# Kernel optimization log

Hardware: AMD Instinct MI355X
Metric: run time of the kernel (lower is better)

The kernel has to match this reference:

```python
import jax, jax.numpy as jnp
import numpy as np

N = 100000
E = 1600000
IN_CH = 128
HEADS = 4
OUT_CH = 32


def setup_inputs() -> dict:
    key = jax.random.key(0)
    k1, k2, k3, k4, k5, k6 = jax.random.split(key, 6)
    x = jax.random.normal(k1, (N, IN_CH), dtype=jnp.float32)
    edge_attr = jax.random.normal(k2, (E,), dtype=jnp.float32)
    edge_index = jax.random.randint(k3, (2, E), 0, N, dtype=jnp.int64)
    # xavier-uniform-ish parameter init
    def xavier(k, shape):
        fan_in, fan_out = shape[-1], shape[-2] if len(shape) > 1 else shape[-1]
        lim = jnp.sqrt(6.0 / (fan_in + fan_out)).astype(jnp.float32)
        return jax.random.uniform(k, shape, jnp.float32, -lim, lim)
    lin_w = xavier(k4, (HEADS * OUT_CH, IN_CH))       # nn.Linear weight [out,in]
    lin_edge_w = xavier(k5, (HEADS * OUT_CH, 1))      # [out,1]
    att = xavier(k6, (1, HEADS, 3 * OUT_CH))
    return {"x": x, "edge_attr": edge_attr, "edge_index": edge_index,
            "lin_w": lin_w, "lin_edge_w": lin_edge_w, "att": att}


def reference(x, edge_attr, edge_index, lin_w, lin_edge_w, att):
    n = x.shape[0]
    # node transform: [N, H, C]
    xh = (x @ lin_w.T).reshape(n, HEADS, OUT_CH)
    # edge transform: [E, H, C]
    eh = (edge_attr[:, None] @ lin_edge_w.T).reshape(-1, HEADS, OUT_CH)
    row, col = edge_index[0], edge_index[1]
    # split att into source/dest/edge parts to avoid materializing cat([x_i,x_j,e])
    att_i, att_j, att_e = jnp.split(att, 3, axis=-1)  # each [1, H, C]
    # per-edge attention logits: [E, H]
    alpha = ((xh[row] * att_i).sum(-1)
             + (xh[col] * att_j).sum(-1)
             + (eh * att_e).sum(-1))
    alpha = jax.nn.leaky_relu(alpha, negative_slope=0.2)
    # segment softmax over destination node (row)
    amax = jax.ops.segment_max(alpha, row, num_segments=n)           # [N, H]
    amax = jnp.where(jnp.isfinite(amax), amax, 0.0)
    ex = jnp.exp(alpha - amax[row])
    den = jax.ops.segment_sum(ex, row, num_segments=n)               # [N, H]
    alpha = ex / (den[row] + 1e-16)
    # weighted message scatter-add: [N, H, C]
    out = jax.ops.segment_sum(alpha[..., None] * xh[col], row, num_segments=n)
    # concat heads
    return out.reshape(n, HEADS * OUT_CH)
```

## Files before the change

### kernel.cpp

```cpp
#include <hip/hip_runtime.h>

#define HEADS 4
#define OUT_CH 32
#define HC 128
#define INC 128
#define CAP 48

typedef __attribute__((ext_vector_type(8))) short bfrag;
typedef __attribute__((ext_vector_type(4))) float ffrag;

union U16 { uint4 u; bfrag f; };

__device__ __forceinline__ unsigned short f2bf(float f) {
  unsigned int u = __float_as_uint(f);
  unsigned int r = (u + 0x7FFFu + ((u >> 16) & 1u)) >> 16;
  return (unsigned short)r;
}

__global__ void prep_kernel(const float* __restrict__ W,
                            const float* __restrict__ lew,
                            const float* __restrict__ att,
                            unsigned short* __restrict__ Wb,
                            float* __restrict__ ce) {
  int tid = threadIdx.x;
#pragma unroll
  for (int t = 0; t < 64; t++) {
    int idx = tid + t * 256;
    Wb[idx] = f2bf(W[idx]);
  }
  if (tid < HEADS) {
    float s = 0.f;
    for (int c = 0; c < OUT_CH; ++c)
      s += lew[tid * OUT_CH + c] * att[tid * 96 + 2 * OUT_CH + c];
    ce[tid] = s;
  }
}

#define APITCH 136
__global__ __launch_bounds__(256) void gemm_build(
    const float* __restrict__ x, const unsigned short* __restrict__ Wb,
    const float* __restrict__ att, const int* __restrict__ ei,
    const float* __restrict__ ea, unsigned short* __restrict__ xhb,
    float* __restrict__ si, float* __restrict__ sj, int* __restrict__ cnt,
    unsigned int* __restrict__ slots, int nrows, int E, int G) {
  __shared__ unsigned short Als[4][16 * APITCH];

  if (blockIdx.x >= G) {
    int e = (blockIdx.x - G) * 256 + threadIdx.x;
    if (e < E) {
      int r = ei[e];
      int c = ei[E + e];
      unsigned int u = __float_as_uint(ea[e]);
      unsigned int word = ((u + 0x10000u) & 0xFFFE0000u) | (unsigned int)c;
      int pos = atomicAdd(&cnt[r], 1);
      if (pos < CAP) slots[(size_t)r * CAP + pos] = word;
    }
    return;
  }

  const int tid = threadIdx.x;
  const int wid = tid >> 6;
  const int lane = tid & 63;
  const int row0 = blockIdx.x * 64 + wid * 16;
  if (row0 >= nrows) return;
  unsigned short* As = &Als[wid][0];

#pragma unroll
  for (int t = 0; t < 8; t++) {
    int idx = t * 64 + lane;
    int r = idx >> 5;
    int q = idx & 31;
    int gr = row0 + r;
    float4 v = make_float4(0.f, 0.f, 0.f, 0.f);
    if (gr < nrows) v = ((const float4*)x)[(size_t)gr * 32 + q];
    unsigned int p0 = ((unsigned int)f2bf(v.y) << 16) | f2bf(v.x);
    unsigned int p1 = ((unsigned int)f2bf(v.w) << 16) | f2bf(v.z);
    *(uint2*)&As[r * APITCH + q * 4] = make_uint2(p0, p1);
  }

  const int m15 = lane & 15;
  const int g = lane >> 4;

  ffrag acc[8];
#pragma unroll
  for (int t = 0; t < 8; t++) acc[t] = (ffrag){0.f, 0.f, 0.f, 0.f};

#pragma unroll
  for (int ks = 0; ks < 4; ks++) {
    U16 a;
    a.u = *(const uint4*)&As[m15 * APITCH + ks * 32 + g * 8];
#pragma unroll
    for (int nt = 0; nt < 8; nt++) {
      U16 b;
      b.u = *(const uint4*)&Wb[(size_t)(nt * 16 + m15) * 128 + ks * 32 + g * 8];
      acc[nt] = __builtin_amdgcn_mfma_f32_16x16x32_bf16(a.f, b.f, acc[nt],
                                                        0, 0, 0);
    }
  }

  float ai[8], aj[8];
#pragma unroll
  for (int t = 0; t < 8; t++) {
    int h = t >> 1, c = (t & 1) * 16 + m15;
    ai[t] = att[h * 96 + c];
    aj[t] = att[h * 96 + 32 + c];
  }
#pragma unroll
  for (int reg = 0; reg < 4; reg++) {
    float ph_i[4], ph_j[4];
#pragma unroll
    for (int h = 0; h < 4; h++) {
      ph_i[h] = acc[2 * h][reg] * ai[2 * h] + acc[2 * h + 1][reg] * ai[2 * h + 1];
      ph_j[h] = acc[2 * h][reg] * aj[2 * h] + acc[2 * h + 1][reg] * aj[2 * h + 1];
    }
#pragma unroll
    for (int off = 8; off >= 1; off >>= 1) {
#pragma unroll
      for (int h = 0; h < 4; h++) {
        ph_i[h] += __shfl_down(ph_i[h], off, 16);
        ph_j[h] += __shfl_down(ph_j[h], off, 16);
      }
    }
    int gr = row0 + g * 4 + reg;
    if (m15 == 0 && gr < nrows) {
#pragma unroll
      for (int h = 0; h < 4; h++) {
        si[(size_t)gr * 4 + h] = ph_i[h];
        sj[(size_t)gr * 4 + h] = ph_j[h];
      }
    }
  }

#pragma unroll
  for (int t = 0; t < 8; t++) {
#pragma unroll
    for (int reg = 0; reg < 4; reg++) {
      int r = g * 4 + reg;
      int n = t * 16 + m15;
      As[r * 128 + n] = f2bf(acc[t][reg]);
    }
  }
  const uint4* src = (const uint4*)As;
#pragma unroll
  for (int t = 0; t < 4; t++) {
    int idx = t * 64 + lane;
    int r = idx >> 4, q = idx & 15;
    int gr = row0 + r;
    if (gr < nrows) ((uint4*)(xhb + (size_t)gr * 128))[q] = src[idx];
  }
}

__global__ __launch_bounds__(256) void gather_kernel(
    const int* __restrict__ cnt, const unsigned int* __restrict__ slots,
    const float* __restrict__ si, const float* __restrict__ sj,
    const float* __restrict__ ce, const unsigned short* __restrict__ xhb,
    float* __restrict__ out, int n) {
  __shared__ int cls[4][CAP];
  __shared__ float wls[4][4][CAP];

  int wid = threadIdx.x >> 6;
  int node = blockIdx.x * 4 + wid;
  if (node >= n) return;
  int lane = threadIdx.x & 63;
  int h = lane >> 4;

  int m = cnt[node];
  if (m > CAP) m = CAP;

  float4 si4 = *(const float4*)(si + (size_t)node * 4);
  float4 ce4 = *(const float4*)ce;

  if (lane < CAP) {
    int c = 0;
    float w0 = 0.f, w1 = 0.f, w2 = 0.f, w3 = 0.f;
    if (lane < m) {
      unsigned int word = slots[(size_t)node * CAP + lane];
      c = word & 0x1FFFF;
      float eaf = __uint_as_float(word & 0xFFFE0000u);
      float4 sjv = *(const float4*)(sj + (size_t)c * 4);
      float t0 = si4.x + sjv.x + eaf * ce4.x;
      float t1 = si4.y + sjv.y + eaf * ce4.y;
      float t2 = si4.z + sjv.z + eaf * ce4.z;
      float t3 = si4.w + sjv.w + eaf * ce4.w;
      t0 = t0 > 0.f ? t0 : 0.2f * t0;
      t1 = t1 > 0.f ? t1 : 0.2f * t1;
      t2 = t2 > 0.f ? t2 : 0.2f * t2;
      t3 = t3 > 0.f ? t3 : 0.2f * t3;
      w0 = __expf(t0);
      w1 = __expf(t1);
      w2 = __expf(t2);
      w3 = __expf(t3);
    }
    cls[wid][lane] = c;
    wls[wid][0][lane] = w0;
    wls[wid][1][lane] = w1;
    wls[wid][2][lane] = w2;
    wls[wid][3][lane] = w3;
  }

  const unsigned short* xb = xhb + lane * 2;
  float acc0 = 0.f, acc1 = 0.f, wsum = 0.f;
  for (int k = 0; k < m; k += 4) {
    int4 cc = *(const int4*)&cls[wid][k];
    float4 wv = *(const float4*)&wls[wid][h][k];
    unsigned int x0 = *(const unsigned int*)(xb + (size_t)cc.x * 128);
    unsigned int x1 = *(const unsigned int*)(xb + (size_t)cc.y * 128);
    unsigned int x2 = *(const unsigned int*)(xb + (size_t)cc.z * 128);
    unsigned int x3 = *(const unsigned int*)(xb + (size_t)cc.w * 128);
    acc0 += wv.x * __uint_as_float(x0 << 16) +
            wv.y * __uint_as_float(x1 << 16) +
            wv.z * __uint_as_float(x2 << 16) +
            wv.w * __uint_as_float(x3 << 16);
    acc1 += wv.x * __uint_as_float(x0 & 0xFFFF0000u) +
            wv.y * __uint_as_float(x1 & 0xFFFF0000u) +
            wv.z * __uint_as_float(x2 & 0xFFFF0000u) +
            wv.w * __uint_as_float(x3 & 0xFFFF0000u);
    wsum += wv.x + wv.y + wv.z + wv.w;
  }

  float inv = 1.0f / (wsum + 1e-16f);
  float2 o;
  o.x = acc0 * inv;
  o.y = acc1 * inv;
  *(float2*)(out + (size_t)node * HC + lane * 2) = o;
}

extern "C" void kernel_launch(void* const* d_in, const int* in_sizes, int n_in,
                              void* d_out, int out_size, void* d_ws,
                              size_t ws_size, hipStream_t stream) {
  const float* x = (const float*)d_in[0];
  const float* edge_attr = (const float*)d_in[1];
  const int* ei = (const int*)d_in[2];
  const float* lin_w = (const float*)d_in[3];
  const float* lew = (const float*)d_in[4];
  const float* att = (const float*)d_in[5];
  float* out = (float*)d_out;

  const int N = in_sizes[0] / INC;
  const int E = in_sizes[1];

  unsigned int* slots = (unsigned int*)d_ws;
  unsigned short* xhb = (unsigned short*)(slots + (size_t)N * CAP);
  float* si = (float*)(xhb + (size_t)N * 128);
  float* sj = si + (size_t)N * 4;
  float* ce = sj + (size_t)N * 4;
  unsigned short* Wb = (unsigned short*)(ce + 16);
  int* cnt = (int*)(Wb + 16384);

  hipMemsetAsync(cnt, 0, (size_t)N * sizeof(int), stream);
  prep_kernel<<<1, 256, 0, stream>>>(lin_w, lew, att, Wb, ce);

  const int G = (N + 63) / 64;
  const int B = (E + 255) / 256;
  gemm_build<<<G + B, 256, 0, stream>>>(x, Wb, att, ei, edge_attr, xhb, si,
                                        sj, cnt, slots, N, E, G);
  gather_kernel<<<(N + 3) / 4, 256, 0, stream>>>(cnt, slots, si, sj, ce, xhb,
                                                 out, N);
}
```

Measured before the change: 298.2 us.

## Bucket edges by destination range into per-XCD queues before slot scatter

Edge-building blocks no longer do scattered atomics into the per-node slot arrays. Each wave instead appends packed (col|attr, row) records to one of 64 queues, keyed by destination-row bucket and block index modulo 8, using one ballot-aggregated atomic per bucket; the queues live in the output buffer as scratch. A new scatter kernel then drains each bucket from blocks that share the same blockIdx&7, so the cnt atomics and slot writes for a given row range should stay within one L2 partition. The hipMemsetAsync is also folded into a multi-block prep kernel. The cost is an extra write and read of roughly 13 MB of queue records plus one more kernel launch.

```diff
diff --git a/kernel.cpp b/kernel.cpp
--- a/kernel.cpp
+++ b/kernel.cpp
@@ -5,6 +5,8 @@
 #define HC 128
 #define INC 128
 #define CAP 48
+#define NB 8
+#define QCAP 32768
 
 typedef __attribute__((ext_vector_type(8))) short bfrag;
 typedef __attribute__((ext_vector_type(4))) float ffrag;
@@ -17,22 +19,33 @@
   return (unsigned short)r;
 }
 
-__global__ void prep_kernel(const float* __restrict__ W,
-                            const float* __restrict__ lew,
-                            const float* __restrict__ att,
-                            unsigned short* __restrict__ Wb,
-                            float* __restrict__ ce) {
+__global__ __launch_bounds__(256) void prep_kernel(
+    const float* __restrict__ W, const float* __restrict__ lew,
+    const float* __restrict__ att, unsigned short* __restrict__ Wb,
+    float* __restrict__ ce, int* __restrict__ cnt, int* __restrict__ qcnt,
+    int N) {
+  int bid = blockIdx.x;
   int tid = threadIdx.x;
-#pragma unroll
-  for (int t = 0; t < 64; t++) {
-    int idx = tid + t * 256;
-    Wb[idx] = f2bf(W[idx]);
-  }
-  if (tid < HEADS) {
-    float s = 0.f;
-    for (int c = 0; c < OUT_CH; ++c)
-      s += lew[tid * OUT_CH + c] * att[tid * 96 + 2 * OUT_CH + c];
-    ce[tid] = s;
+  if (bid < 16) {
+    int i4 = bid * 256 + tid;
+    float4 v = ((const float4*)W)[i4];
+    ushort4 o;
+    o.x = f2bf(v.x);
+    o.y = f2bf(v.y);
+    o.z = f2bf(v.z);
+    o.w = f2bf(v.w);
+    ((ushort4*)Wb)[i4] = o;
+    if (bid == 0 && tid < HEADS) {
+      float s = 0.f;
+      for (int c = 0; c < OUT_CH; ++c)
+        s += lew[tid * OUT_CH + c] * att[tid * 96 + 2 * OUT_CH + c];
+      ce[tid] = s;
+    }
+  } else {
+    int zi = (bid - 16) * 256 + tid;
+    int stride = (gridDim.x - 16) * 256;
+    for (int i = zi; i < N; i += stride) cnt[i] = 0;
+    if (zi < 64) qcnt[zi] = 0;
   }
 }
 
@@ -41,19 +54,42 @@
     const float* __restrict__ x, const unsigned short* __restrict__ Wb,
     const float* __restrict__ att, const int* __restrict__ ei,
     const float* __restrict__ ea, unsigned short* __restrict__ xhb,
-    float* __restrict__ si, float* __restrict__ sj, int* __restrict__ cnt,
-    unsigned int* __restrict__ slots, int nrows, int E, int G) {
+    float* __restrict__ si, float* __restrict__ sj, int* __restrict__ qcnt,
+    unsigned long long* __restrict__ queue, int nrows, int E, int G,
+    int bsz) {
   __shared__ unsigned short Als[4][16 * APITCH];
 
   if (blockIdx.x >= G) {
     int e = (blockIdx.x - G) * 256 + threadIdx.x;
-    if (e < E) {
+    int lane = threadIdx.x & 63;
+    bool valid = e < E;
+    int b = -1;
+    unsigned long long rec = 0;
+    if (valid) {
       int r = ei[e];
       int c = ei[E + e];
       unsigned int u = __float_as_uint(ea[e]);
       unsigned int word = ((u + 0x10000u) & 0xFFFE0000u) | (unsigned int)c;
-      int pos = atomicAdd(&cnt[r], 1);
-      if (pos < CAP) slots[(size_t)r * CAP + pos] = word;
+      rec = ((unsigned long long)word << 32) | (unsigned int)r;
+      b = r / bsz;
+      if (b > NB - 1) b = NB - 1;
+    }
+    int xs = blockIdx.x & 7;
+#pragma unroll
+    for (int bb = 0; bb < NB; ++bb) {
+      unsigned long long mask = __ballot(valid && (b == bb));
+      if (mask == 0) continue;
+      int nsel = __popcll(mask);
+      int leader = __ffsll((unsigned long long)mask) - 1;
+      int base = 0;
+      if (lane == leader) base = atomicAdd(&qcnt[xs * NB + bb], nsel);
+      base = __shfl(base, leader);
+      if (valid && b == bb) {
+        int rank = __popcll(mask & ((1ull << lane) - 1ull));
+        int pos = base + rank;
+        if (pos < QCAP)
+          queue[((size_t)(xs * NB + bb) << 15) + pos] = rec;
+      }
     }
     return;
   }
@@ -91,9 +127,9 @@
     a.u = *(const uint4*)&As[m15 * APITCH + ks * 32 + g * 8];
 #pragma unroll
     for (int nt = 0; nt < 8; nt++) {
-      U16 b;
-      b.u = *(const uint4*)&Wb[(size_t)(nt * 16 + m15) * 128 + ks * 32 + g * 8];
-      acc[nt] = __builtin_amdgcn_mfma_f32_16x16x32_bf16(a.f, b.f, acc[nt],
+      U16 bfr;
+      bfr.u = *(const uint4*)&Wb[(size_t)(nt * 16 + m15) * 128 + ks * 32 + g * 8];
+      acc[nt] = __builtin_amdgcn_mfma_f32_16x16x32_bf16(a.f, bfr.f, acc[nt],
                                                         0, 0, 0);
     }
   }
@@ -147,6 +183,28 @@
     int r = idx >> 4, q = idx & 15;
     int gr = row0 + r;
     if (gr < nrows) ((uint4*)(xhb + (size_t)gr * 128))[q] = src[idx];
+  }
+}
+
+__global__ __launch_bounds__(256) void scatter_kernel(
+    const unsigned long long* __restrict__ queue, const int* __restrict__ qcnt,
+    int* __restrict__ cnt, unsigned int* __restrict__ slots) {
+  int b = blockIdx.x & 7;
+  int chunk = blockIdx.x >> 3;
+  int nchunk = gridDim.x >> 3;
+#pragma unroll
+  for (int xs = 0; xs < NB; ++xs) {
+    int qi = xs * NB + b;
+    int m = qcnt[qi];
+    if (m > QCAP) m = QCAP;
+    const unsigned long long* q = queue + ((size_t)qi << 15);
+    for (int i = chunk * 256 + threadIdx.x; i < m; i += nchunk * 256) {
+      unsigned long long rec = q[i];
+      int r = (int)(unsigned int)rec;
+      unsigned int word = (unsigned int)(rec >> 32);
+      int pos = atomicAdd(&cnt[r], 1);
+      if (pos < CAP) slots[(size_t)r * CAP + pos] = word;
+    }
   }
 }
 
@@ -246,14 +304,18 @@
   float* ce = sj + (size_t)N * 4;
   unsigned short* Wb = (unsigned short*)(ce + 16);
   int* cnt = (int*)(Wb + 16384);
-
-  hipMemsetAsync(cnt, 0, (size_t)N * sizeof(int), stream);
-  prep_kernel<<<1, 256, 0, stream>>>(lin_w, lew, att, Wb, ce);
+  int* qcnt = cnt + N;
+  unsigned long long* queue = (unsigned long long*)d_out;
+
+  const int bsz = (N + NB - 1) / NB;
+
+  prep_kernel<<<128, 256, 0, stream>>>(lin_w, lew, att, Wb, ce, cnt, qcnt, N);
 
   const int G = (N + 63) / 64;
   const int B = (E + 255) / 256;
   gemm_build<<<G + B, 256, 0, stream>>>(x, Wb, att, ei, edge_attr, xhb, si,
-                                        sj, cnt, slots, N, E, G);
+                                        sj, qcnt, queue, N, E, G, bsz);
+  scatter_kernel<<<2048, 256, 0, stream>>>(queue, qcnt, cnt, slots);
   gather_kernel<<<(N + 3) / 4, 256, 0, stream>>>(cnt, slots, si, sj, ce, xhb,
                                                  out, N);
 }
```

New measurement: 977.2 us. 3.28x slower.
